# Kernel tuning notes

Measured on AMD Instinct MI355X. Metric: run time of the kernel, lower is better.

## Reference

```python
import jax, jax.numpy as jnp
import numpy as np
from functools import partial

SLOPE = 25.0
BETA1 = float(np.exp(-1.0 / 5.0))   # tau_mso_ms=5, dt=1
BETA2 = float(np.exp(-1.0 / 10.0))  # tau_ic_ms=10, dt=1
THR1 = 1.0
THR2 = 1.0

@jax.custom_vjp
def spike_fn(x):
    # Heaviside forward, fast_sigmoid surrogate backward
    return (x > 0).astype(x.dtype)

def _spike_fwd(x):
    return spike_fn(x), x

def _spike_bwd(x, g):
    return (g / (SLOPE * jnp.abs(x) + 1.0) ** 2,)

spike_fn.defvjp(_spike_fwd, _spike_bwd)

def setup_inputs() -> dict:
    key = jax.random.key(0)
    ks = jax.random.split(key, 10)
    T, B, I, H1, H2 = 500, 256, 128, 512, 256
    spikes = (jax.random.uniform(ks[0], (T, B, I)) < 0.2).astype(jnp.float32)
    def lin(k, o, i):
        s = 1.0 / np.sqrt(i)
        k1, k2 = jax.random.split(k)
        return (jax.random.uniform(k1, (o, i), minval=-s, maxval=s).astype(jnp.float32),
                jax.random.uniform(k2, (o,), minval=-s, maxval=s).astype(jnp.float32))
    W1, b1 = lin(ks[1], H1, I)
    W2, b2 = lin(ks[2], H2, H1)
    Wr, br = lin(ks[3], 2, H2)
    Ws, bs = lin(ks[4], 2, H1)
    return {"spikes": spikes, "W1": W1, "b1": b1, "W2": W2, "b2": b2,
            "Wr": Wr, "br": br, "Ws": Ws, "bs": bs}

def _lif_step(beta, thr, mem, cur):
    # snntorch Leaky, reset_mechanism='subtract': reset from incoming mem (detached)
    reset = jax.lax.stop_gradient((mem > thr).astype(mem.dtype))
    mem = beta * mem + cur - reset * thr
    spk = spike_fn(mem - thr)
    return mem, spk

def reference(spikes, W1, b1, W2, b2, Wr, br, Ws, bs):
    T, B, _ = spikes.shape
    H1, H2 = W1.shape[0], W2.shape[0]
    cur1 = jnp.einsum('tbi,hi->tbh', spikes, W1) + b1  # [T,B,H1]

    def step1(mem, c):
        mem, spk = _lif_step(BETA1, THR1, mem, c)
        return mem, spk
    _, spk1 = jax.lax.scan(step1, jnp.zeros((B, H1), spikes.dtype), cur1)  # [T,B,H1]

    cur2 = jnp.einsum('tbh,gh->tbg', spk1, W2) + b2  # [T,B,H2]

    def step2(carry, c):
        mem, msum = carry
        mem, spk = _lif_step(BETA2, THR2, mem, c)
        return (mem, msum + mem), spk
    (_, mem2_sum), spk2 = jax.lax.scan(
        step2, (jnp.zeros((B, H2), spikes.dtype), jnp.zeros((B, H2), spikes.dtype)), cur2)

    inv_t = 1.0 / T
    mem2_avg = mem2_sum * inv_t
    spk1_avg = spk1.mean(axis=0)
    out = mem2_avg @ Wr.T + br + spk1_avg @ Ws.T + bs  # [B,2]
    spk1_mean = spk1.mean()
    spk2_mean = spk2.mean()
    return out, spk1_mean, spk2_mean
```

## Files before the change

kernel.cpp:

```cpp
#include <hip/hip_runtime.h>
#include <hip/hip_bf16.h>
#include <hip/hip_fp16.h>

typedef __attribute__((ext_vector_type(8))) short short8;
typedef __attribute__((ext_vector_type(4))) short short4v;
typedef __attribute__((ext_vector_type(8))) _Float16 f16x8;
typedef __attribute__((ext_vector_type(4))) _Float16 f16x4;
typedef __attribute__((ext_vector_type(4))) float f32x4;

static constexpr int NIN  = 128;
static constexpr int NH1  = 512;
static constexpr int NH2  = 256;
static constexpr float LO_SCALE = 4096.0f;
static constexpr float LO_INV   = 2.44140625e-4f;
static constexpr float BETA1 = 0.8187307530779818f;
static constexpr float BETA2 = 0.9048374180359595f;

__device__ __forceinline__ unsigned short f2h_bits(float x) {
    _Float16 h = (_Float16)x;
    unsigned short u;
    __builtin_memcpy(&u, &h, 2);
    return u;
}
__device__ __forceinline__ float h2f(unsigned short u) {
    _Float16 h;
    __builtin_memcpy(&h, &u, 2);
    return (float)h;
}

__device__ __forceinline__ void gload16(const unsigned short* g, unsigned short* l) {
    __builtin_amdgcn_global_load_lds(
        (const __attribute__((address_space(1))) unsigned int*)(g),
        (__attribute__((address_space(3))) unsigned int*)(l),
        16, 0, 0);
}

__global__ __launch_bounds__(256) void prep_weights(
    const float* __restrict__ W1, const float* __restrict__ W2,
    unsigned short* __restrict__ w1s,
    unsigned short* __restrict__ w2s,
    unsigned int* __restrict__ cnt1, unsigned int* __restrict__ cnt2)
{
    int idx = blockIdx.x * 256 + threadIdx.x;
    if (idx == 0) { cnt1[0] = 0u; cnt2[0] = 0u; }
    const int n1 = NH1 * NIN;
    const int n2 = NH2 * NH1;
    if (idx < n1) {
        float w = W1[idx];
        unsigned short hi = f2h_bits(w);
        float r = (w - h2f(hi)) * LO_SCALE;
        unsigned short lo = f2h_bits(r);
        w1s[idx] = hi; w1s[n1 + idx] = lo;
    }
    if (idx < n2) {
        float w = W2[idx];
        unsigned short hi = f2h_bits(w);
        float r = (w - h2f(hi)) * LO_SCALE;
        unsigned short lo = f2h_bits(r);
        w2s[idx] = hi; w2s[n2 + idx] = lo;
    }
}

__global__ __launch_bounds__(256) void pack_spikes(
    const float* __restrict__ sp, unsigned long long* __restrict__ bits)
{
    int i = blockIdx.x * 256 + threadIdx.x;
    bool b = sp[i] != 0.0f;
    unsigned long long m = __ballot(b);
    if ((threadIdx.x & 63) == 0) bits[i >> 6] = m;
}

__device__ __forceinline__ void load_abytes(
    const unsigned char* __restrict__ Ab, int j, int bg, int wr, int lr, int lk,
    unsigned int a[2][4])
{
#pragma unroll
    for (int rb = 0; rb < 2; ++rb) {
        int row = wr * 32 + rb * 16 + lr;
        int t = j * 16 + (row >> 2); if (t > 499) t = 499;
        int gr = t * 256 + bg * 4 + (row & 3);
#pragma unroll
        for (int ks = 0; ks < 4; ++ks)
            a[rb][ks] = Ab[(size_t)gr * 16 + ks * 4 + lk];
    }
}

__global__ __launch_bounds__(256) void fused1(
    const unsigned char* __restrict__ Ab,
    const unsigned short* __restrict__ w1s,
    const float* __restrict__ bias,
    unsigned long long* __restrict__ spkb,
    float* __restrict__ s1sum,
    unsigned int* __restrict__ cnt_g)
{
    __shared__ __align__(16) float tile[64 * 66];
    __shared__ __align__(16) unsigned short lut4[64];

    const int tid = threadIdx.x;
    const int bg  = blockIdx.x;
    const int ht  = blockIdx.y;
    const int h0  = ht * 64;

    if (tid < 16) {
        short4v e;
#pragma unroll
        for (int i = 0; i < 4; ++i)
            e[i] = ((tid >> i) & 1) ? (short)0x3C00 : (short)0;
        *reinterpret_cast<short4v*>(&lut4[tid * 4]) = e;
    }

    const int w = tid >> 6, lane = tid & 63, lr = lane & 15, lk = lane >> 4;
    const int wr = w >> 1, wc = w & 1;

    f16x8 bH[2][4], bL[2][4];
#pragma unroll
    for (int cb = 0; cb < 2; ++cb)
#pragma unroll
        for (int ks = 0; ks < 4; ++ks) {
            int col = h0 + wc * 32 + cb * 16 + lr;
            bH[cb][ks] = *reinterpret_cast<const f16x8*>(
                w1s + col * 128 + ks * 32 + lk * 8);
            bL[cb][ks] = *reinterpret_cast<const f16x8*>(
                w1s + 65536 + col * 128 + ks * 32 + lk * 8);
        }
    float bcol[2];
#pragma unroll
    for (int cb = 0; cb < 2; ++cb) bcol[cb] = bias[h0 + wc * 32 + cb * 16 + lr];

    const int sb = tid >> 6;
    const int sh = tid & 63;
    float mem = 0.f, sv = 0.f;
    int cnt = 0;

    unsigned int a_cur[2][4], a_nxt[2][4];
    load_abytes(Ab, 0, bg, wr, lr, lk, a_cur);
    __syncthreads();

    for (int j = 0; j < 32; ++j) {
        if (j < 31) load_abytes(Ab, j + 1, bg, wr, lr, lk, a_nxt);

        f32x4 aH[2][2], aL[2][2];
#pragma unroll
        for (int a = 0; a < 2; ++a)
#pragma unroll
            for (int b = 0; b < 2; ++b) {
                aH[a][b] = (f32x4){0.f, 0.f, 0.f, 0.f};
                aL[a][b] = (f32x4){0.f, 0.f, 0.f, 0.f};
            }
#pragma unroll
        for (int ks = 0; ks < 4; ++ks) {
            f16x8 af[2];
#pragma unroll
            for (int rb = 0; rb < 2; ++rb) {
                unsigned int by = a_cur[rb][ks];
                f16x4 lo = *reinterpret_cast<const f16x4*>(&lut4[(by & 15u) * 4]);
                f16x4 hi = *reinterpret_cast<const f16x4*>(&lut4[((by >> 4) & 15u) * 4]);
                af[rb] = __builtin_shufflevector(lo, hi, 0, 1, 2, 3, 4, 5, 6, 7);
            }
#pragma unroll
            for (int cb = 0; cb < 2; ++cb)
#pragma unroll
                for (int rb = 0; rb < 2; ++rb) {
                    aH[rb][cb] = __builtin_amdgcn_mfma_f32_16x16x32_f16(
                        af[rb], bH[cb][ks], aH[rb][cb], 0, 0, 0);
                    aL[rb][cb] = __builtin_amdgcn_mfma_f32_16x16x32_f16(
                        af[rb], bL[cb][ks], aL[rb][cb], 0, 0, 0);
                }
        }
#pragma unroll
        for (int cb = 0; cb < 2; ++cb) {
            int col = wc * 32 + cb * 16 + lr;
#pragma unroll
            for (int rb = 0; rb < 2; ++rb) {
                int rbase = wr * 32 + rb * 16 + lk * 4;
#pragma unroll
                for (int jj = 0; jj < 4; ++jj)
                    tile[(rbase + jj) * 66 + col] =
                        fmaf(aL[rb][cb][jj], LO_INV, aH[rb][cb][jj]) + bcol[cb];
            }
        }
        __syncthreads();

        float cv[16];
#pragma unroll
        for (int tl = 0; tl < 16; ++tl)
            cv[tl] = tile[(tl * 4 + sb) * 66 + sh];
#pragma unroll
        for (int tl = 0; tl < 16; ++tl) {
            int t = j * 16 + tl;
            if (t < 500) {
                mem = BETA1 * mem + cv[tl] - sv;
                bool spk = mem > 1.f;
                sv = spk ? 1.f : 0.f;
                cnt += (int)spk;
                unsigned long long B = __ballot(spk);
                if (sh == 0)
                    spkb[(size_t)(t * 256 + bg * 4 + sb) * 8 + ht] = B;
            }
        }
        __syncthreads();

        if (j < 31) {
#pragma unroll
            for (int rb = 0; rb < 2; ++rb)
#pragma unroll
                for (int ks = 0; ks < 4; ++ks) a_cur[rb][ks] = a_nxt[rb][ks];
        }
    }

    s1sum[(bg * 4 + sb) * 512 + h0 + sh] = (float)cnt;
    int rc = cnt;
#pragma unroll
    for (int off = 32; off > 0; off >>= 1) rc += __shfl_down(rc, off);
    if (sh == 0) atomicAdd(cnt_g, (unsigned int)rc);
}

template<int N, int K>
__global__ __launch_bounds__(256) void gemm_bits(
    const unsigned char* __restrict__ Ab,
    const unsigned short* __restrict__ Bs,
    const float* __restrict__ bias,
    float* __restrict__ C,
    int M)
{
    constexpr int NK = N * K;
    constexpr int nk = K / 32;
    constexpr int kb = K / 8;

    __shared__ __align__(16) unsigned short Bsh[3][8192];
    __shared__ __align__(16) unsigned short lut4[64];

    const int tid  = threadIdx.x;
    const int w    = tid >> 6;
    const int lane = tid & 63;
    const int lr   = lane & 15;
    const int lk   = lane >> 4;
    const int wr   = w >> 1;
    const int wc   = w & 1;

    if (tid < 16) {
        short4v e;
#pragma unroll
        for (int i = 0; i < 4; ++i)
            e[i] = ((tid >> i) & 1) ? (short)0x3C00 : (short)0;
        *reinterpret_cast<short4v*>(&lut4[tid * 4]) = e;
    }
    asm volatile("s_waitcnt lgkmcnt(0)" ::: "memory");

    const int m0 = blockIdx.x * 128;
    const int n0 = blockIdx.y * 128;
    const int ulog = ((lane & 3) ^ ((lane >> 3) & 3)) * 8;

    int gBoff[4], lBoff[4];
#pragma unroll
    for (int j = 0; j < 4; ++j) {
        int i = w * 4 + j;
        int s = i >> 3, blk = i & 7;
        int row = blk * 16 + (lane >> 2);
        gBoff[j] = s * NK + (n0 + row) * K + ulog;
        lBoff[j] = s * 4096 + blk * 512;
    }
    const unsigned char* aptr[4];
#pragma unroll
    for (int rb = 0; rb < 4; ++rb)
        aptr[rb] = Ab + (size_t)(m0 + wr * 64 + rb * 16 + lr) * kb + lk;

    f32x4 accH[4][4], accL[4][4];
#pragma unroll
    for (int i = 0; i < 4; ++i)
#pragma unroll
        for (int j = 0; j < 4; ++j) {
            accH[i][j] = (f32x4){0.f, 0.f, 0.f, 0.f};
            accL[i][j] = (f32x4){0.f, 0.f, 0.f, 0.f};
        }

    unsigned int ab[3][4];
#pragma unroll
    for (int p = 0; p < 2; ++p) {
#pragma unroll
        for (int j = 0; j < 4; ++j)
            gload16(Bs + gBoff[j] + p * 32, &Bsh[p][lBoff[j]]);
#pragma unroll
        for (int rb = 0; rb < 4; ++rb)
            ab[p][rb] = aptr[rb][p * 4];
    }

#pragma unroll
    for (int ks = 0; ks < nk; ++ks) {
        if (ks + 1 < nk) {
            asm volatile("s_waitcnt vmcnt(8)" ::: "memory");
        } else {
            asm volatile("s_waitcnt vmcnt(0)" ::: "memory");
        }
        __builtin_amdgcn_s_barrier();
        __builtin_amdgcn_sched_barrier(0);

        if (ks + 2 < nk) {
#pragma unroll
            for (int j = 0; j < 4; ++j)
                gload16(Bs + gBoff[j] + (ks + 2) * 32, &Bsh[(ks + 2) % 3][lBoff[j]]);
#pragma unroll
            for (int rb = 0; rb < 4; ++rb)
                ab[(ks + 2) % 3][rb] = aptr[rb][(ks + 2) * 4];
        }
        __builtin_amdgcn_sched_barrier(0);

        f16x8 af[4];
#pragma unroll
        for (int rb = 0; rb < 4; ++rb) {
            unsigned int b = ab[ks % 3][rb];
            f16x4 lo = *reinterpret_cast<const f16x4*>(&lut4[(b & 15u) * 4]);
            f16x4 hi = *reinterpret_cast<const f16x4*>(&lut4[((b >> 4) & 15u) * 4]);
            af[rb] = __builtin_shufflevector(lo, hi, 0, 1, 2, 3, 4, 5, 6, 7);
        }

#pragma unroll
        for (int cb = 0; cb < 4; ++cb) {
            int row = wc * 64 + cb * 16 + lr;
            int u = (lk ^ ((row >> 1) & 3)) * 8;
            f16x8 bfH = *reinterpret_cast<const f16x8*>(&Bsh[ks % 3][row * 32 + u]);
            f16x8 bfL = *reinterpret_cast<const f16x8*>(&Bsh[ks % 3][4096 + row * 32 + u]);
#pragma unroll
            for (int rb = 0; rb < 4; ++rb) {
                accH[rb][cb] = __builtin_amdgcn_mfma_f32_16x16x32_f16(
                    af[rb], bfH, accH[rb][cb], 0, 0, 0);
                accL[rb][cb] = __builtin_amdgcn_mfma_f32_16x16x32_f16(
                    af[rb], bfL, accL[rb][cb], 0, 0, 0);
            }
        }
    }

#pragma unroll
    for (int cb = 0; cb < 4; ++cb) {
        int col = n0 + wc * 64 + cb * 16 + lr;
        float bv = bias[col];
#pragma unroll
        for (int rb = 0; rb < 4; ++rb) {
            int row = m0 + wr * 64 + rb * 16 + lk * 4;
#pragma unroll
            for (int j = 0; j < 4; ++j)
                C[(size_t)(row + j) * N + col] =
                    fmaf(accL[rb][cb][j], LO_INV, accH[rb][cb][j]) + bv;
        }
    }
}

__global__ __launch_bounds__(256) void scan2(
    const float* __restrict__ cur,
    float* __restrict__ msum_o,
    unsigned int* __restrict__ cnt_g)
{
    int tid = blockIdx.x * 256 + threadIdx.x;
    float mem = 0.f, sv = 0.f, ms = 0.f;
    int cnt = 0;
    const float* base = cur + tid;

    float c[10], n[10];
#pragma unroll
    for (int i = 0; i < 10; ++i) c[i] = base[(size_t)i * 65536];

    for (int g = 0; g < 50; ++g) {
        if (g < 49) {
#pragma unroll
            for (int i = 0; i < 10; ++i)
                n[i] = base[(size_t)((g + 1) * 10 + i) * 65536];
        }
#pragma unroll
        for (int i = 0; i < 10; ++i) {
            mem = BETA2 * mem + c[i] - sv;
            ms += mem;
            bool b = mem > 1.f;
            sv = b ? 1.f : 0.f;
            cnt += (int)b;
        }
#pragma unroll
        for (int i = 0; i < 10; ++i) c[i] = n[i];
    }
    msum_o[tid] = ms;
    int rc = cnt;
#pragma unroll
    for (int off = 32; off > 0; off >>= 1) rc += __shfl_down(rc, off);
    if ((threadIdx.x & 63) == 0) atomicAdd(cnt_g, (unsigned int)rc);
}

__global__ __launch_bounds__(256) void readout(
    const float* __restrict__ msum, const float* __restrict__ s1sum,
    const float* __restrict__ Wr, const float* __restrict__ br,
    const float* __restrict__ Ws, const float* __restrict__ bs,
    const unsigned int* __restrict__ cnt1, const unsigned int* __restrict__ cnt2,
    float* __restrict__ out)
{
    __shared__ float r0[256], r1[256];
    int b = blockIdx.x, t = threadIdx.x;
    const float inv_t = 1.0f / 500.0f;
    float m  = msum[b * 256 + t] * inv_t;
    float p0 = m * Wr[t];
    float p1 = m * Wr[256 + t];
    float sa = s1sum[b * 512 + t] * inv_t;
    float sb = s1sum[b * 512 + 256 + t] * inv_t;
    p0 += sa * Ws[t]       + sb * Ws[256 + t];
    p1 += sa * Ws[512 + t] + sb * Ws[768 + t];
    r0[t] = p0; r1[t] = p1;
    __syncthreads();
    for (int st = 128; st > 0; st >>= 1) {
        if (t < st) { r0[t] += r0[t + st]; r1[t] += r1[t + st]; }
        __syncthreads();
    }
    if (t == 0) {
        out[b * 2 + 0] = r0[0] + br[0] + bs[0];
        out[b * 2 + 1] = r1[0] + br[1] + bs[1];
        if (b == 0) {
            out[512] = (float)cnt1[0] * (1.0f / 65536000.0f);
            out[513] = (float)cnt2[0] * (1.0f / 32768000.0f);
        }
    }
}

extern "C" void kernel_launch(void* const* d_in, const int* in_sizes, int n_in,
                              void* d_out, int out_size, void* d_ws, size_t ws_size,
                              hipStream_t stream) {
    const float* spikes = (const float*)d_in[0];
    const float* W1 = (const float*)d_in[1];
    const float* b1 = (const float*)d_in[2];
    const float* W2 = (const float*)d_in[3];
    const float* b2 = (const float*)d_in[4];
    const float* Wr = (const float*)d_in[5];
    const float* br = (const float*)d_in[6];
    const float* Ws = (const float*)d_in[7];
    const float* bs = (const float*)d_in[8];
    float* out = (float*)d_out;

    char* wsb = (char*)d_ws;
    size_t o = 0;
    unsigned short* w1s = (unsigned short*)(wsb + o); o += (size_t)2 * 65536 * 2;
    unsigned short* w2s = (unsigned short*)(wsb + o); o += (size_t)2 * 131072 * 2;
    unsigned long long* spbits = (unsigned long long*)(wsb + o); o += (size_t)256000 * 8;
    unsigned long long* spkb   = (unsigned long long*)(wsb + o); o += (size_t)1024000 * 8;
    float* cur2 = (float*)(wsb + o);                  o += (size_t)500 * 65536 * 4;
    float* s1sum = (float*)(wsb + o); o += 524288;
    float* msum  = (float*)(wsb + o); o += 262144;
    unsigned int* cnt1 = (unsigned int*)(wsb + o); o += 256;
    unsigned int* cnt2 = (unsigned int*)(wsb + o); o += 256;

    prep_weights<<<512, 256, 0, stream>>>(W1, W2, w1s, w2s, cnt1, cnt2);
    pack_spikes<<<64000, 256, 0, stream>>>(spikes, spbits);

    fused1<<<dim3(64, 8), 256, 0, stream>>>(
        (const unsigned char*)spbits, w1s, b1, spkb, s1sum, cnt1);

    gemm_bits<NH2, NH1><<<dim3(1000, 2), 256, 0, stream>>>(
        (const unsigned char*)spkb, w2s, b2, cur2, 128000);

    scan2<<<256, 256, 0, stream>>>(cur2, msum, cnt2);

    readout<<<256, 256, 0, stream>>>(msum, s1sum, Wr, br, Ws, bs, cnt1, cnt2, out);
}
```

Baseline: 261.5 us.

## Double-buffer LIF1 tile to overlap MFMA of next chunk with scan

Software-pipelines the fused layer-1 kernel. The GEMM for chunk j+1 is issued while the LIF recurrence for chunk j runs, using a double-buffered shared tile, which removes one of the two barriers per iteration. The row mapping is changed so each lane's 16 rows are consecutive timesteps of one batch. The tile is also stored transposed with a stride of 68, so the scan reads timesteps as f32x4 vectors. A-operand loads are prefetched two chunks ahead. The cost is more shared memory and register pressure.

```diff
diff --git a/kernel.cpp b/kernel.cpp
--- a/kernel.cpp
+++ b/kernel.cpp
@@ -70,18 +70,17 @@
     if ((threadIdx.x & 63) == 0) bits[i >> 6] = m;
 }
 
-__device__ __forceinline__ void load_abytes(
-    const unsigned char* __restrict__ Ab, int j, int bg, int wr, int lr, int lk,
-    unsigned int a[2][4])
-{
-#pragma unroll
-    for (int rb = 0; rb < 2; ++rb) {
-        int row = wr * 32 + rb * 16 + lr;
-        int t = j * 16 + (row >> 2); if (t > 499) t = 499;
-        int gr = t * 256 + bg * 4 + (row & 3);
-#pragma unroll
-        for (int ks = 0; ks < 4; ++ks)
-            a[rb][ks] = Ab[(size_t)gr * 16 + ks * 4 + lk];
+__device__ __forceinline__ void load_a1(
+    const unsigned char* __restrict__ Ab, int j, int lr, int lk,
+    const int bidx0, const int bidx1, unsigned int (&a)[2][4])
+{
+    int t = j * 16 + lr; if (t > 499) t = 499;
+    size_t b0 = ((size_t)t * 256 + bidx0) * 16 + lk;
+    size_t b1 = ((size_t)t * 256 + bidx1) * 16 + lk;
+#pragma unroll
+    for (int ks = 0; ks < 4; ++ks) {
+        a[0][ks] = Ab[b0 + ks * 4];
+        a[1][ks] = Ab[b1 + ks * 4];
     }
 }
 
@@ -93,7 +92,7 @@
     float* __restrict__ s1sum,
     unsigned int* __restrict__ cnt_g)
 {
-    __shared__ __align__(16) float tile[64 * 66];
+    __shared__ __align__(16) float tile[2][64 * 68];
     __shared__ __align__(16) unsigned short lut4[64];
 
     const int tid = threadIdx.x;
@@ -127,85 +126,136 @@
 #pragma unroll
     for (int cb = 0; cb < 2; ++cb) bcol[cb] = bias[h0 + wc * 32 + cb * 16 + lr];
 
+    const int bidx0 = bg * 4 + 2 * wr;
+    const int bidx1 = bidx0 + 1;
+
     const int sb = tid >> 6;
     const int sh = tid & 63;
     float mem = 0.f, sv = 0.f;
     int cnt = 0;
 
-    unsigned int a_cur[2][4], a_nxt[2][4];
-    load_abytes(Ab, 0, bg, wr, lr, lk, a_cur);
+    f32x4 accH[2][2], accL[2][2];
+#pragma unroll
+    for (int a = 0; a < 2; ++a)
+#pragma unroll
+        for (int b = 0; b < 2; ++b) {
+            accH[a][b] = (f32x4){0.f, 0.f, 0.f, 0.f};
+            accL[a][b] = (f32x4){0.f, 0.f, 0.f, 0.f};
+        }
+
+    unsigned int a_cur[2][4], a_fut[2][4];
+    load_a1(Ab, 0, lr, lk, bidx0, bidx1, a_cur);
     __syncthreads();
 
+#pragma unroll
+    for (int ks = 0; ks < 4; ++ks) {
+        f16x8 af[2];
+#pragma unroll
+        for (int rb = 0; rb < 2; ++rb) {
+            unsigned int by = a_cur[rb][ks];
+            f16x4 lo = *reinterpret_cast<const f16x4*>(&lut4[(by & 15u) * 4]);
+            f16x4 hi = *reinterpret_cast<const f16x4*>(&lut4[((by >> 4) & 15u) * 4]);
+            af[rb] = __builtin_shufflevector(lo, hi, 0, 1, 2, 3, 4, 5, 6, 7);
+        }
+#pragma unroll
+        for (int cb = 0; cb < 2; ++cb)
+#pragma unroll
+            for (int rb = 0; rb < 2; ++rb) {
+                accH[rb][cb] = __builtin_amdgcn_mfma_f32_16x16x32_f16(
+                    af[rb], bH[cb][ks], accH[rb][cb], 0, 0, 0);
+                accL[rb][cb] = __builtin_amdgcn_mfma_f32_16x16x32_f16(
+                    af[rb], bL[cb][ks], accL[rb][cb], 0, 0, 0);
+            }
+    }
+#pragma unroll
+    for (int cb = 0; cb < 2; ++cb) {
+#pragma unroll
+        for (int rb = 0; rb < 2; ++rb) {
+            int col = wc * 32 + cb * 16 + lr;
+            int row = (2 * wr + rb) * 16 + lk * 4;
+            f32x4 v;
+#pragma unroll
+            for (int jj = 0; jj < 4; ++jj)
+                v[jj] = fmaf(accL[rb][cb][jj], LO_INV, accH[rb][cb][jj]) + bcol[cb];
+            *reinterpret_cast<f32x4*>(&tile[0][col * 68 + row]) = v;
+            accH[rb][cb] = (f32x4){0.f, 0.f, 0.f, 0.f};
+            accL[rb][cb] = (f32x4){0.f, 0.f, 0.f, 0.f};
+        }
+    }
+    load_a1(Ab, 1, lr, lk, bidx0, bidx1, a_cur);
+    __syncthreads();
+
     for (int j = 0; j < 32; ++j) {
-        if (j < 31) load_abytes(Ab, j + 1, bg, wr, lr, lk, a_nxt);
-
-        f32x4 aH[2][2], aL[2][2];
-#pragma unroll
-        for (int a = 0; a < 2; ++a)
-#pragma unroll
-            for (int b = 0; b < 2; ++b) {
-                aH[a][b] = (f32x4){0.f, 0.f, 0.f, 0.f};
-                aL[a][b] = (f32x4){0.f, 0.f, 0.f, 0.f};
+        if (j + 2 < 32) load_a1(Ab, j + 2, lr, lk, bidx0, bidx1, a_fut);
+
+        f32x4 cv[4];
+#pragma unroll
+        for (int q = 0; q < 4; ++q)
+            cv[q] = *reinterpret_cast<const f32x4*>(
+                &tile[j & 1][sh * 68 + sb * 16 + q * 4]);
+
+        if (j < 31) {
+#pragma unroll
+            for (int ks = 0; ks < 4; ++ks) {
+                f16x8 af[2];
+#pragma unroll
+                for (int rb = 0; rb < 2; ++rb) {
+                    unsigned int by = a_cur[rb][ks];
+                    f16x4 lo = *reinterpret_cast<const f16x4*>(&lut4[(by & 15u) * 4]);
+                    f16x4 hi = *reinterpret_cast<const f16x4*>(&lut4[((by >> 4) & 15u) * 4]);
+                    af[rb] = __builtin_shufflevector(lo, hi, 0, 1, 2, 3, 4, 5, 6, 7);
+                }
+#pragma unroll
+                for (int cb = 0; cb < 2; ++cb)
+#pragma unroll
+                    for (int rb = 0; rb < 2; ++rb) {
+                        accH[rb][cb] = __builtin_amdgcn_mfma_f32_16x16x32_f16(
+                            af[rb], bH[cb][ks], accH[rb][cb], 0, 0, 0);
+                        accL[rb][cb] = __builtin_amdgcn_mfma_f32_16x16x32_f16(
+                            af[rb], bL[cb][ks], accL[rb][cb], 0, 0, 0);
+                    }
             }
-#pragma unroll
-        for (int ks = 0; ks < 4; ++ks) {
-            f16x8 af[2];
-#pragma unroll
-            for (int rb = 0; rb < 2; ++rb) {
-                unsigned int by = a_cur[rb][ks];
-                f16x4 lo = *reinterpret_cast<const f16x4*>(&lut4[(by & 15u) * 4]);
-                f16x4 hi = *reinterpret_cast<const f16x4*>(&lut4[((by >> 4) & 15u) * 4]);
-                af[rb] = __builtin_shufflevector(lo, hi, 0, 1, 2, 3, 4, 5, 6, 7);
+        }
+
+#pragma unroll
+        for (int q = 0; q < 4; ++q) {
+#pragma unroll
+            for (int i = 0; i < 4; ++i) {
+                int t = j * 16 + q * 4 + i;
+                if (t < 500) {
+                    mem = BETA1 * mem + cv[q][i] - sv;
+                    bool spk = mem > 1.f;
+                    sv = spk ? 1.f : 0.f;
+                    cnt += (int)spk;
+                    unsigned long long B = __ballot(spk);
+                    if (sh == 0)
+                        spkb[(size_t)(t * 256 + bg * 4 + sb) * 8 + ht] = B;
+                }
             }
-#pragma unroll
-            for (int cb = 0; cb < 2; ++cb)
+        }
+
+        if (j < 31) {
+#pragma unroll
+            for (int cb = 0; cb < 2; ++cb) {
 #pragma unroll
                 for (int rb = 0; rb < 2; ++rb) {
-                    aH[rb][cb] = __builtin_amdgcn_mfma_f32_16x16x32_f16(
-                        af[rb], bH[cb][ks], aH[rb][cb], 0, 0, 0);
-                    aL[rb][cb] = __builtin_amdgcn_mfma_f32_16x16x32_f16(
-                        af[rb], bL[cb][ks], aL[rb][cb], 0, 0, 0);
+                    int col = wc * 32 + cb * 16 + lr;
+                    int row = (2 * wr + rb) * 16 + lk * 4;
+                    f32x4 v;
+#pragma unroll
+                    for (int jj = 0; jj < 4; ++jj)
+                        v[jj] = fmaf(accL[rb][cb][jj], LO_INV, accH[rb][cb][jj]) + bcol[cb];
+                    *reinterpret_cast<f32x4*>(&tile[(j + 1) & 1][col * 68 + row]) = v;
+                    accH[rb][cb] = (f32x4){0.f, 0.f, 0.f, 0.f};
+                    accL[rb][cb] = (f32x4){0.f, 0.f, 0.f, 0.f};
                 }
-        }
-#pragma unroll
-        for (int cb = 0; cb < 2; ++cb) {
-            int col = wc * 32 + cb * 16 + lr;
-#pragma unroll
-            for (int rb = 0; rb < 2; ++rb) {
-                int rbase = wr * 32 + rb * 16 + lk * 4;
-#pragma unroll
-                for (int jj = 0; jj < 4; ++jj)
-                    tile[(rbase + jj) * 66 + col] =
-                        fmaf(aL[rb][cb][jj], LO_INV, aH[rb][cb][jj]) + bcol[cb];
             }
+#pragma unroll
+            for (int rb = 0; rb < 2; ++rb)
+#pragma unroll
+                for (int ks = 0; ks < 4; ++ks) a_cur[rb][ks] = a_fut[rb][ks];
         }
         __syncthreads();
-
-        float cv[16];
-#pragma unroll
-        for (int tl = 0; tl < 16; ++tl)
-            cv[tl] = tile[(tl * 4 + sb) * 66 + sh];
-#pragma unroll
-        for (int tl = 0; tl < 16; ++tl) {
-            int t = j * 16 + tl;
-            if (t < 500) {
-                mem = BETA1 * mem + cv[tl] - sv;
-                bool spk = mem > 1.f;
-                sv = spk ? 1.f : 0.f;
-                cnt += (int)spk;
-                unsigned long long B = __ballot(spk);
-                if (sh == 0)
-                    spkb[(size_t)(t * 256 + bg * 4 + sb) * 8 + ht] = B;
-            }
-        }
-        __syncthreads();
-
-        if (j < 31) {
-#pragma unroll
-            for (int rb = 0; rb < 2; ++rb)
-#pragma unroll
-                for (int ks = 0; ks < 4; ++ks) a_cur[rb][ks] = a_nxt[rb][ks];
-        }
     }
 
     s1sum[(bg * 4 + sb) * 512 + h0 + sh] = (float)cnt;
```

New measurement: 263.2 us. No clear change (+0.7%).
